# Optimization experiments

Hardware: AMD Instinct MI355X
Metric: run time of the kernel (lower is better)

Reference implementation:

```python
import math
import jax, jax.numpy as jnp
import numpy as np

B, T, C = 256, 200, 512
H = 8
N_ATTN = 512
HEAD = N_ATTN // H          # 64
ROT = HEAD // 2             # 32 (rotary_ndims = head_size * 0.5)
MAXLEN = 200
ITEM_NUM = 100000


def setup_inputs() -> dict:
    key = jax.random.key(0)
    ks = jax.random.split(key, 16)
    s = 0.02
    item_emb = jax.random.normal(ks[0], (ITEM_NUM + 1, C), jnp.float32) * s
    item_emb = item_emb.at[0].set(0.0)  # padding_idx=0
    inp = {
        "user_ids": jax.random.randint(ks[1], (B,), 0, 10000),
        "log_seqs": jax.random.randint(ks[2], (B, T), 0, ITEM_NUM + 1),
        "pos_seqs": jax.random.randint(ks[3], (B, T), 0, ITEM_NUM + 1),
        "neg_seqs": jax.random.randint(ks[4], (B, T), 0, ITEM_NUM + 1),
        "item_emb": item_emb,
        "time_w": 1.0 + jax.random.normal(ks[5], (H, MAXLEN), jnp.float32) * 0.1,
        "time_alpha": 1.0 + jax.random.normal(ks[6], (H, 1, MAXLEN), jnp.float32) * 0.1,
        "time_beta": 1.0 + jax.random.normal(ks[7], (H, MAXLEN, 1), jnp.float32) * 0.1,
        "time_gamma": 1.0 + jax.random.normal(ks[8], (MAXLEN, 1), jnp.float32) * 0.1,
        "Wq": jax.random.normal(ks[9], (N_ATTN, C), jnp.float32) * s,
        "bq": jnp.zeros((N_ATTN,), jnp.float32),
        "Wk": jax.random.normal(ks[10], (N_ATTN, C), jnp.float32) * s,
        "bk": jnp.zeros((N_ATTN,), jnp.float32),
        "Wv": jax.random.normal(ks[11], (N_ATTN, C), jnp.float32) * s,
        "bv": jnp.zeros((N_ATTN,), jnp.float32),
        "Wmix": jax.random.normal(ks[12], (H, H), jnp.float32) * (1.0 / math.sqrt(H)),
        "Wo": jax.random.normal(ks[13], (C, N_ATTN), jnp.float32) * s,
        "bo": jnp.zeros((C,), jnp.float32),
    }
    return inp


def _rotate_half(x):
    x1, x2 = x[..., : x.shape[-1] // 2], x[..., x.shape[-1] // 2 :]
    return jnp.concatenate((-x2, x1), axis=-1)


def _mha_pro(x_items, time_w, time_alpha, time_beta, time_gamma,
             Wq, bq, Wk, bk, Wv, bv, Wmix, Wo, bo):
    # x_items: [B, T, C]
    TT = MAXLEN
    # Toeplitz time-decay matrix built exactly like the torch pad/tile/reshape trick
    w = jnp.pad(time_w, ((0, 0), (0, TT)))          # [H, 2TT]
    w = jnp.tile(w, (1, TT))                         # [H, 2TT*TT]
    w = w[:, :-TT].reshape(H, TT, 2 * TT - 1)        # [H, TT, 2TT-1]
    w = w[:, :, TT - 1 :]                            # [H, TT, TT]
    w = w[:, :T, :T] * time_alpha[:, :, :T] * time_beta[:, :T, :]  # [H, T, T]

    # time_shift: shift first half of channels down by one token
    half = C // 2
    shifted = jnp.pad(x_items[:, :, :half], ((0, 0), (1, 0), (0, 0)))[:, :-1]
    x = jnp.concatenate([shifted, x_items[:, :, half:]], axis=-1)  # [B, T, C]

    q = (x @ Wq.T + bq).reshape(B, T, H, HEAD).transpose(0, 2, 1, 3)  # [B,H,T,D]
    k = (x @ Wk.T + bk).reshape(B, T, H, HEAD).transpose(0, 2, 1, 3)
    v = (x @ Wv.T + bv).reshape(B, T, H, HEAD).transpose(0, 2, 1, 3)

    # partial rotary on first ROT dims
    q_rot, q_pass = q[..., :ROT], q[..., ROT:]
    k_rot, k_pass = k[..., :ROT], k[..., ROT:]
    inv_freq = 1.0 / (10000.0 ** (jnp.arange(0, ROT, 2, dtype=jnp.float32) / ROT))
    freqs = jnp.arange(T, dtype=jnp.float32)[:, None] * inv_freq[None, :]  # [T, ROT/2]
    emb = jnp.concatenate((freqs, freqs), axis=-1)   # [T, ROT]
    cos, sin = jnp.cos(emb), jnp.sin(emb)
    q_rot = q_rot * cos + _rotate_half(q_rot) * sin
    k_rot = k_rot * cos + _rotate_half(k_rot) * sin
    q = jnp.concatenate((q_rot, q_pass), axis=-1)
    k = jnp.concatenate((k_rot, k_pass), axis=-1)

    att = jnp.einsum('bhtd,bhsd->bhts', q, k) * (1.0 / math.sqrt(HEAD))
    causal = jnp.tril(jnp.ones((T, T), bool))
    att = jnp.where(causal, att, -jnp.inf)
    att = jax.nn.softmax(att, axis=-1)
    att = att * w                                   # learned time-decay mask
    att = jnp.einsum('hg,bgts->bhts', Wmix, att)    # 1x1 conv across heads

    out = jnp.einsum('bhts,bhsd->bhtd', att, v)
    out = out.transpose(0, 2, 1, 3).reshape(B, T, N_ATTN)
    out = (out @ Wo.T + bo) * time_gamma[:T, :]
    return out


def reference(user_ids, log_seqs, pos_seqs, neg_seqs, item_emb,
              time_w, time_alpha, time_beta, time_gamma,
              Wq, bq, Wk, bk, Wv, bv, Wmix, Wo, bo):
    x_items = item_emb[log_seqs]                    # [B, T, C]
    log_feats = _mha_pro(x_items, time_w, time_alpha, time_beta, time_gamma,
                         Wq, bq, Wk, bk, Wv, bv, Wmix, Wo, bo)
    pos_embs = item_emb[pos_seqs]
    neg_embs = item_emb[neg_seqs]
    pos_logits = log_feats * pos_embs               # [B, T, C] (as in source)
    neg_logits = (log_feats * neg_embs).sum(axis=-1)  # [B, T]
    return pos_logits, neg_logits
```

## Files before the change

kernel.cpp:

```cpp
#include <hip/hip_runtime.h>

#define B_    256
#define T_    200
#define C_    512
#define H_    8
#define HEAD_ 64
#define M_    (B_ * T_)
#define POS_OUT_ (M_ * C_)
#define QK_ROWS_ 208
#define VT_PAD_  224
#define P_PAD_   208

typedef __attribute__((ext_vector_type(8))) _Float16 f16x8;
typedef __attribute__((ext_vector_type(4))) _Float16 f16x4;
typedef __attribute__((ext_vector_type(2))) _Float16 f16x2;
typedef __attribute__((ext_vector_type(4))) float f32x4;

__device__ __forceinline__ void gload16(const void* g, void* l) {
    __builtin_amdgcn_global_load_lds(
        (const __attribute__((address_space(1))) unsigned int*)g,
        (__attribute__((address_space(3))) unsigned int*)l, 16, 0, 0);
}

__global__ __launch_bounds__(256) void gather_shift_k(
    const float* __restrict__ emb, const int* __restrict__ logs,
    _Float16* __restrict__ x)
{
    int bt = blockIdx.x;
    int t  = bt % T_;
    int tid = threadIdx.x;
    int c  = tid * 2;
    _Float16* xr = x + (size_t)bt * C_;
    if (c < 256) {
        if (t == 0) {
            *(f16x2*)(xr + c) = (f16x2){(_Float16)0.0f, (_Float16)0.0f};
        } else {
            int id_prev = logs[bt - 1];
            float2 v = *(const float2*)(emb + (size_t)id_prev * C_ + c);
            *(f16x2*)(xr + c) = (f16x2){(_Float16)v.x, (_Float16)v.y};
        }
    } else {
        int id_cur = logs[bt];
        float2 v = *(const float2*)(emb + (size_t)id_cur * C_ + c);
        *(f16x2*)(xr + c) = (f16x2){(_Float16)v.x, (_Float16)v.y};
    }
}

__global__ __launch_bounds__(256) void convert_w_k(
    const float* __restrict__ Wq, const float* __restrict__ Wk,
    const float* __restrict__ Wv, const float* __restrict__ Wo,
    _Float16* __restrict__ dst)
{
    int idx = blockIdx.x * 256 + threadIdx.x;
    int mat = idx >> 16;
    int off = (idx & 65535) << 2;
    const float* src = (mat == 0) ? Wq : (mat == 1) ? Wk : (mat == 2) ? Wv : Wo;
    float4 v = *(const float4*)(src + off);
    f16x4 o = { (_Float16)v.x, (_Float16)v.y, (_Float16)v.z, (_Float16)v.w };
    *(f16x4*)(dst + ((size_t)mat << 18) + off) = o;
}

__global__ __launch_bounds__(256) void wtab_k(
    const float* __restrict__ tw, const float* __restrict__ ta,
    const float* __restrict__ tb, float* __restrict__ wtab)
{
    int idx = blockIdx.x * 256 + threadIdx.x;
    int g   = idx / (208 * 208);
    int rem = idx % (208 * 208);
    int t = rem / 208, s = rem % 208;
    int tt = min(t, 199), ss = min(s, 199);
    int wi = min(max(199 - tt + ss, 0), 199);
    wtab[idx] = tw[g * 200 + wi] * ta[g * 200 + ss] * tb[g * 200 + tt];
}

__global__ __launch_bounds__(256) void zero_pads_k(
    _Float16* __restrict__ Qb, _Float16* __restrict__ Kb,
    _Float16* __restrict__ Vt)
{
    int bh = blockIdx.x;
    int tid = threadIdx.x;
    for (int idx = tid; idx < 8 * 64; idx += 256) {
        Qb[(size_t)bh * QK_ROWS_ * 64 + 200 * 64 + idx] = (_Float16)0.0f;
        Kb[(size_t)bh * QK_ROWS_ * 64 + 200 * 64 + idx] = (_Float16)0.0f;
    }
    for (int idx = tid; idx < 64 * (VT_PAD_ - 200); idx += 256) {
        int d = idx / (VT_PAD_ - 200), s = 200 + idx % (VT_PAD_ - 200);
        Vt[(size_t)bh * 64 * VT_PAD_ + (size_t)d * VT_PAD_ + s] = (_Float16)0.0f;
    }
}

__global__ __launch_bounds__(256) void gemm_qkv_k(
    const _Float16* __restrict__ xh,
    const _Float16* __restrict__ Wh,
    const float* __restrict__ bq, const float* __restrict__ bk, const float* __restrict__ bv,
    _Float16* __restrict__ Qb, _Float16* __restrict__ Kb,
    _Float16* __restrict__ Vt,
    int nmt)
{
    int n = blockIdx.x;
    int mt, v;
    if ((nmt & 7) == 0) { int q8 = n & 7, i = n >> 3; mt = (i / 12) * 8 + q8; v = i % 12; }
    else               { mt = n / 12; v = n % 12; }
    int which = v >> 2;
    int nt    = v & 3;
    int m0    = mt * 128;
    const _Float16* Wm = Wh + ((size_t)(which * 4 + nt) * 128) * 512;
    const float* bias = (which == 0) ? bq : (which == 1) ? bk : bv;

    __shared__ _Float16 As[3][128 * 32];
    __shared__ _Float16 Bs[3][128 * 32];

    int tid  = threadIdx.x;
    int w    = tid >> 6, lane = tid & 63;
    int quad = lane >> 4, l15 = lane & 15;
    int wm   = w >> 1,    wn  = w & 1;
    int srow = lane >> 2, scg = lane & 3;
    int scg_src = scg ^ ((srow >> 1) & 3);
    int rq = (l15 >> 1) & 3;

    auto stage = [&](int buf, int k0) {
#pragma unroll
        for (int rr = 0; rr < 2; ++rr) {
            int seg = rr * 4 + w;
            int row = seg * 16 + srow;
            gload16(xh + (size_t)(m0 + row) * 512 + k0 + scg_src * 8, As[buf] + seg * 512);
            gload16(Wm + (size_t)row * 512 + k0 + scg_src * 8, Bs[buf] + seg * 512);
        }
    };

    f32x4 acc[4][4];
#pragma unroll
    for (int m = 0; m < 4; ++m)
#pragma unroll
        for (int nn = 0; nn < 4; ++nn) acc[m][nn] = (f32x4){0.f, 0.f, 0.f, 0.f};

    stage(0, 0);
    stage(1, 32);
#pragma unroll
    for (int s = 0; s < 16; ++s) {
        if (s < 15) asm volatile("s_waitcnt vmcnt(4)" ::: "memory");
        else        asm volatile("s_waitcnt vmcnt(0)" ::: "memory");
        __builtin_amdgcn_s_barrier();
        __builtin_amdgcn_sched_barrier(0);
        const _Float16* Ab = As[s % 3];
        const _Float16* Bb = Bs[s % 3];
        f16x8 af[4], bf[4];
#pragma unroll
        for (int m = 0; m < 4; ++m)
            af[m] = *(const f16x8*)(Ab + (wm * 4 + m) * 512 + l15 * 32 + (quad ^ rq) * 8);
#pragma unroll
        for (int nn = 0; nn < 4; ++nn)
            bf[nn] = *(const f16x8*)(Bb + (wn * 4 + nn) * 512 + l15 * 32 + (quad ^ rq) * 8);
        if (s <= 13) stage((s + 2) % 3, (s + 2) * 32);
#pragma unroll
        for (int m = 0; m < 4; ++m)
#pragma unroll
            for (int nn = 0; nn < 4; ++nn)
                acc[m][nn] = __builtin_amdgcn_mfma_f32_16x16x32_f16(af[m], bf[nn], acc[m][nn], 0, 0, 0);
    }

    int h = nt * 2 + wn;
    if (which < 2) {
        _Float16* dst = (which == 0) ? Qb : Kb;
        float sc = (which == 0) ? 0.125f : 1.0f;
        float invf = powf(10000.0f, -(float)l15 / 16.0f);
#pragma unroll
        for (int m = 0; m < 4; ++m) {
#pragma unroll
            for (int r = 0; r < 4; ++r) {
                int row = m0 + wm * 64 + m * 16 + quad * 4 + r;
                int bl = row / T_, t = row % T_;
                float sn, cs;
                __sincosf((float)t * invf, &sn, &cs);
                size_t base = ((size_t)(bl * 8 + h) * QK_ROWS_ + t) * 64;
                float av = acc[m][0][r] + bias[h * 64 + l15];
                float bv2 = acc[m][1][r] + bias[h * 64 + 16 + l15];
                dst[base + l15]      = (_Float16)((av * cs - bv2 * sn) * sc);
                dst[base + 16 + l15] = (_Float16)((bv2 * cs + av * sn) * sc);
                dst[base + 32 + l15] = (_Float16)((acc[m][2][r] + bias[h * 64 + 32 + l15]) * sc);
                dst[base + 48 + l15] = (_Float16)((acc[m][3][r] + bias[h * 64 + 48 + l15]) * sc);
            }
        }
    } else {
#pragma unroll
        for (int nn = 0; nn < 4; ++nn) {
            int ch = nn * 16 + l15;
            float bval = bias[h * 64 + ch];
#pragma unroll
            for (int m = 0; m < 4; ++m) {
                int r0 = m0 + wm * 64 + m * 16 + quad * 4;
                int t0v = r0 % T_;
                if (t0v <= 196) {
                    int bl = r0 / T_;
                    f16x4 v4 = {(_Float16)(acc[m][nn][0] + bval),
                                (_Float16)(acc[m][nn][1] + bval),
                                (_Float16)(acc[m][nn][2] + bval),
                                (_Float16)(acc[m][nn][3] + bval)};
                    *(f16x4*)(Vt + ((size_t)(bl * 8 + h) * 64 + ch) * VT_PAD_ + t0v) = v4;
                } else {
#pragma unroll
                    for (int r = 0; r < 4; ++r) {
                        int rw = r0 + r;
                        int bl = rw / T_, s = rw % T_;
                        Vt[((size_t)(bl * 8 + h) * 64 + ch) * VT_PAD_ + s] = (_Float16)(acc[m][nn][r] + bval);
                    }
                }
            }
        }
    }
}

__global__ __launch_bounds__(512) void attn_fused_k(
    const _Float16* __restrict__ Qb, const _Float16* __restrict__ Kb,
    const _Float16* __restrict__ Vt,
    const float* __restrict__ wtab,
    const float* __restrict__ wmix,
    _Float16* __restrict__ ao)
{
    int n    = blockIdx.x;
    int xcd  = n & 7, slot = n >> 3;
    int i_tile = slot % 13;
    int b      = (slot / 13) * 8 + xcd;

    int tid  = threadIdx.x;
    int wave = tid >> 6, lane = tid & 63;
    int quad = lane >> 4, l15 = lane & 15;
    int t0   = i_tile * 16;
    int nst  = i_tile + 1;
    int smax = nst * 16;

    __shared__ _Float16 Pt[8][16][P_PAD_];
    __shared__ float mixs[64];

    if (tid < 64) mixs[tid] = wmix[tid];
    __syncthreads();

    {
        int g = wave;
        const _Float16* Qg = Qb + (size_t)(b * 8 + g) * QK_ROWS_ * 64;
        const _Float16* Kg = Kb + (size_t)(b * 8 + g) * QK_ROWS_ * 64;
        f16x8 a0 = *(const f16x8*)(Qg + (size_t)(t0 + l15) * 64 + quad * 8);
        f16x8 a1 = *(const f16x8*)(Qg + (size_t)(t0 + l15) * 64 + quad * 8 + 32);

        f32x4 sf[13];
        __builtin_amdgcn_s_setprio(1);
#pragma unroll
        for (int st = 0; st < 13; ++st) if (st < nst) {
            f16x8 k0 = *(const f16x8*)(Kg + (size_t)(st * 16 + l15) * 64 + quad * 8);
            f16x8 k1 = *(const f16x8*)(Kg + (size_t)(st * 16 + l15) * 64 + quad * 8 + 32);
            f32x4 c = {0.f, 0.f, 0.f, 0.f};
            c = __builtin_amdgcn_mfma_f32_16x16x32_f16(a0, k0, c, 0, 0, 0);
            c = __builtin_amdgcn_mfma_f32_16x16x32_f16(a1, k1, c, 0, 0, 0);
            sf[st] = c;
        }
        __builtin_amdgcn_s_setprio(0);
        float inv[4];
#pragma unroll
        for (int r = 0; r < 4; ++r) {
            int t = t0 + quad * 4 + r;
            float sum = 0.f;
#pragma unroll
            for (int st = 0; st < 13; ++st) {
                if (st < nst - 1) {
                    float e = __expf(sf[st][r]); sf[st][r] = e; sum += e;
                } else if (st == nst - 1) {
                    int s = t0 + l15;
                    float e = (s <= t) ? __expf(sf[st][r]) : 0.f;
                    sf[st][r] = e; sum += e;
                }
            }
            sum += __shfl_xor(sum, 1);
            sum += __shfl_xor(sum, 2);
            sum += __shfl_xor(sum, 4);
            sum += __shfl_xor(sum, 8);
            inv[r] = 1.0f / sum;
        }
        const float* wg = wtab + ((size_t)g * 208 + t0) * 208;
#pragma unroll
        for (int st = 0; st < 13; ++st) if (st < nst) {
            int s = st * 16 + l15;
#pragma unroll
            for (int r = 0; r < 4; ++r) {
                int trow = quad * 4 + r;
                float wv = wg[trow * 208 + s];
                Pt[g][trow][s] = (_Float16)(sf[st][r] * inv[r] * wv);
            }
        }
    }
    __syncthreads();

    {
        f16x2 mx[64];
#pragma unroll
        for (int i = 0; i < 64; ++i) {
            _Float16 mh = (_Float16)mixs[i];
            mx[i] = (f16x2){mh, mh};
        }
        int nitems = smax << 3;
        for (int idx = tid; idx < nitems; idx += 512) {
            int tloc = idx & 15;
            int sp   = (idx >> 4) << 1;
            f16x2 pv[8];
#pragma unroll
            for (int g = 0; g < 8; ++g) pv[g] = *(const f16x2*)&Pt[g][tloc][sp];
#pragma unroll
            for (int ho = 0; ho < 8; ++ho) {
                f16x2 o = mx[ho * 8] * pv[0];
#pragma unroll
                for (int g = 1; g < 8; ++g) o += mx[ho * 8 + g] * pv[g];
                *(f16x2*)&Pt[ho][tloc][sp] = o;
            }
        }
    }
    __syncthreads();

    {
        int nk = (nst + 1) >> 1;
        int hda = wave;
        const _Float16* Vh = Vt + (size_t)(b * 8 + hda) * 64 * VT_PAD_;
        f32x4 c4[4];
#pragma unroll
        for (int n2 = 0; n2 < 4; ++n2) c4[n2] = (f32x4){0.f, 0.f, 0.f, 0.f};
        __builtin_amdgcn_s_setprio(1);
#pragma unroll
        for (int ks = 0; ks < 7; ++ks) if (ks < nk) {
            int cc = ks * 32 + quad * 8;
            bool oob = cc >= smax;
            int cl = oob ? 0 : cc;
            f16x8 a = *(const f16x8*)(&Pt[hda][l15][cl]);
            if (oob) {
#pragma unroll
                for (int j = 0; j < 8; ++j) a[j] = (_Float16)0.0f;
            }
#pragma unroll
            for (int n2 = 0; n2 < 4; ++n2) {
                f16x8 bb = *(const f16x8*)(Vh + (size_t)(n2 * 16 + l15) * VT_PAD_ + ks * 32 + quad * 8);
                c4[n2] = __builtin_amdgcn_mfma_f32_16x16x32_f16(a, bb, c4[n2], 0, 0, 0);
            }
        }
        __builtin_amdgcn_s_setprio(0);
#pragma unroll
        for (int n2 = 0; n2 < 4; ++n2)
#pragma unroll
            for (int r = 0; r < 4; ++r) {
                int t = t0 + quad * 4 + r;
                if (t < 200)
                    ao[((size_t)(b * T_ + t)) * 512 + hda * 64 + n2 * 16 + l15] = (_Float16)c4[n2][r];
            }
    }
}

__global__ __launch_bounds__(256) void gemm_out_k(
    const _Float16* __restrict__ Ah, const _Float16* __restrict__ Woh,
    const float* __restrict__ bo, const float* __restrict__ gamma,
    float* __restrict__ dst, int nmt)
{
    int n = blockIdx.x;
    int mt, nt;
    if ((nmt & 7) == 0) { int q8 = n & 7, i = n >> 3; mt = (i / 4) * 8 + q8; nt = i % 4; }
    else               { mt = n / 4; nt = n % 4; }
    int m0 = mt * 128;
    const _Float16* Wm = Woh + (size_t)nt * 128 * 512;

    __shared__ _Float16 As[3][128 * 32];
    __shared__ _Float16 Bs[3][128 * 32];

    int tid  = threadIdx.x;
    int w    = tid >> 6, lane = tid & 63;
    int quad = lane >> 4, l15 = lane & 15;
    int wm   = w >> 1,    wn  = w & 1;
    int srow = lane >> 2, scg = lane & 3;
    int scg_src = scg ^ ((srow >> 1) & 3);
    int rq = (l15 >> 1) & 3;

    auto stage = [&](int buf, int k0) {
#pragma unroll
        for (int rr = 0; rr < 2; ++rr) {
            int seg = rr * 4 + w;
            int row = seg * 16 + srow;
            gload16(Ah + (size_t)(m0 + row) * 512 + k0 + scg_src * 8, As[buf] + seg * 512);
            gload16(Wm + (size_t)row * 512 + k0 + scg_src * 8, Bs[buf] + seg * 512);
        }
    };

    f32x4 acc[4][4];
#pragma unroll
    for (int m = 0; m < 4; ++m)
#pragma unroll
        for (int nn = 0; nn < 4; ++nn) acc[m][nn] = (f32x4){0.f, 0.f, 0.f, 0.f};

    stage(0, 0);
    stage(1, 32);
#pragma unroll
    for (int s = 0; s < 16; ++s) {
        if (s < 15) asm volatile("s_waitcnt vmcnt(4)" ::: "memory");
        else        asm volatile("s_waitcnt vmcnt(0)" ::: "memory");
        __builtin_amdgcn_s_barrier();
        __builtin_amdgcn_sched_barrier(0);
        const _Float16* Ab = As[s % 3];
        const _Float16* Bb = Bs[s % 3];
        f16x8 af[4], bf[4];
#pragma unroll
        for (int m = 0; m < 4; ++m)
            af[m] = *(const f16x8*)(Ab + (wm * 4 + m) * 512 + l15 * 32 + (quad ^ rq) * 8);
#pragma unroll
        for (int nn = 0; nn < 4; ++nn)
            bf[nn] = *(const f16x8*)(Bb + (wn * 4 + nn) * 512 + l15 * 32 + (quad ^ rq) * 8);
        if (s <= 13) stage((s + 2) % 3, (s + 2) * 32);
#pragma unroll
        for (int m = 0; m < 4; ++m)
#pragma unroll
            for (int nn = 0; nn < 4; ++nn)
                acc[m][nn] = __builtin_amdgcn_mfma_f32_16x16x32_f16(af[m], bf[nn], acc[m][nn], 0, 0, 0);
    }

#pragma unroll
    for (int m = 0; m < 4; ++m)
#pragma unroll
        for (int nn = 0; nn < 4; ++nn)
#pragma unroll
            for (int r = 0; r < 4; ++r) {
                int row = m0 + wm * 64 + m * 16 + quad * 4 + r;
                int col = nt * 128 + wn * 64 + nn * 16 + l15;
                dst[(size_t)row * 512 + col] = (acc[m][nn][r] + bo[col]) * gamma[row % T_];
            }
}

__global__ __launch_bounds__(256) void logits_k(
    const float* __restrict__ lf, const float* __restrict__ emb,
    const int* __restrict__ pos, const int* __restrict__ neg,
    float* __restrict__ out, int bt0)
{
    int wid = threadIdx.x >> 6, lane = threadIdx.x & 63;
    int bt = blockIdx.x * 4 + wid;
    const float* l  = lf  + (size_t)bt * 512;
    const float* pe = emb + (size_t)pos[bt] * 512;
    const float* ne = emb + (size_t)neg[bt] * 512;
    float* po = out + (size_t)(bt0 + bt) * 512;
    float nacc = 0.f;
#pragma unroll
    for (int rep = 0; rep < 2; ++rep) {
        int i4 = (lane + rep * 64) * 4;
        float4 lv = *(const float4*)(l  + i4);
        float4 pv = *(const float4*)(pe + i4);
        float4 nv = *(const float4*)(ne + i4);
        float4 ov;
        ov.x = lv.x * pv.x; ov.y = lv.y * pv.y;
        ov.z = lv.z * pv.z; ov.w = lv.w * pv.w;
        *(float4*)(po + i4) = ov;
        nacc += lv.x * nv.x + lv.y * nv.y + lv.z * nv.z + lv.w * nv.w;
    }
#pragma unroll
    for (int off = 32; off >= 1; off >>= 1) nacc += __shfl_xor(nacc, off);
    if (lane == 0)
        out[(size_t)POS_OUT_ + bt0 + bt] = nacc;
}

extern "C" void kernel_launch(void* const* d_in, const int* in_sizes, int n_in,
                              void* d_out, int out_size, void* d_ws, size_t ws_size,
                              hipStream_t stream)
{
    const int* logs = (const int*)d_in[1];
    const int* pos  = (const int*)d_in[2];
    const int* neg  = (const int*)d_in[3];
    const float* emb = (const float*)d_in[4];
    const float* tw  = (const float*)d_in[5];
    const float* ta  = (const float*)d_in[6];
    const float* tb  = (const float*)d_in[7];
    const float* tg  = (const float*)d_in[8];
    const float* Wq  = (const float*)d_in[9];
    const float* bq  = (const float*)d_in[10];
    const float* Wk  = (const float*)d_in[11];
    const float* bk  = (const float*)d_in[12];
    const float* Wv  = (const float*)d_in[13];
    const float* bv  = (const float*)d_in[14];
    const float* wmix= (const float*)d_in[15];
    const float* Wo  = (const float*)d_in[16];
    const float* bo  = (const float*)d_in[17];

    const size_t PER_B = (size_t)T_ * C_ * 2
                       + (size_t)8 * QK_ROWS_ * 64 * 2
                       + (size_t)8 * QK_ROWS_ * 64 * 2
                       + (size_t)8 * 64 * VT_PAD_ * 2
                       + (size_t)T_ * C_ * 2
                       + (size_t)T_ * C_ * 4;
    const size_t SZ_WH = (size_t)4 * 512 * 512 * 2;
    const size_t SZ_WT = (size_t)8 * 208 * 208 * 4;

    int CB = (ws_size >= SZ_WH + SZ_WT + PER_B * B_) ? B_ : 32;
    int nch = B_ / CB;
    int CM = CB * T_;
    int NMT = CM / 128;

    char* p = (char*)d_ws;
    _Float16*       Wh   = (_Float16*)p;  p += SZ_WH;
    float*          wtab = (float*)p;     p += SZ_WT;
    _Float16*       xh   = (_Float16*)p;  p += (size_t)CM * C_ * 2;
    _Float16*       Qb   = (_Float16*)p;  p += (size_t)CB * 8 * QK_ROWS_ * 64 * 2;
    _Float16*       Kb   = (_Float16*)p;  p += (size_t)CB * 8 * QK_ROWS_ * 64 * 2;
    _Float16*       Vt   = (_Float16*)p;  p += (size_t)CB * 8 * 64 * VT_PAD_ * 2;
    _Float16*       aoh  = (_Float16*)p;  p += (size_t)CM * C_ * 2;
    float*          lf   = (float*)p;

    convert_w_k<<<1024, 256, 0, stream>>>(Wq, Wk, Wv, Wo, Wh);
    wtab_k<<<1352, 256, 0, stream>>>(tw, ta, tb, wtab);
    zero_pads_k<<<CB * 8, 256, 0, stream>>>(Qb, Kb, Vt);

    for (int c = 0; c < nch; ++c) {
        int bt0 = c * CM;
        gather_shift_k<<<CM, 256, 0, stream>>>(emb, logs + bt0, xh);
        gemm_qkv_k<<<NMT * 12, 256, 0, stream>>>(xh, Wh, bq, bk, bv, Qb, Kb, Vt, NMT);
        attn_fused_k<<<13 * CB, 512, 0, stream>>>(Qb, Kb, Vt, wtab, wmix, aoh);
        gemm_out_k<<<NMT * 4, 256, 0, stream>>>(aoh, Wh + (size_t)3 * 512 * 512, bo, tg, lf, NMT);
        logits_k<<<CM / 4, 256, 0, stream>>>(lf, emb, pos + bt0, neg + bt0, (float*)d_out, bt0);
    }
}
```

Measured before the change: 700.2 us.

## Fuse logits into output GEMM epilogue and prefetch K/V in attention

The separate logits kernel is removed. Its work moves into the gemm_out epilogue: pos logits are written directly, and neg logits are reduced with shuffles and accumulated with atomicAdd into an output region that a new kernel zeroes first. This avoids writing and re-reading the fp32 log_feats buffer. In the attention kernel the next K and V fragments are software-prefetched, the P LDS row padding changes, launch bounds gain a minimum-occupancy hint, and a barrier is dropped. The risks are less coalesced epilogue stores, atomic contention, higher register pressure, and a possible race on the shared mix weights.

Measured after the change: 689.5 us. About the same (-1.5%).

```diff
diff --git a/kernel.cpp b/kernel.cpp
--- a/kernel.cpp
+++ b/kernel.cpp
@@ -9,7 +9,7 @@
 #define POS_OUT_ (M_ * C_)
 #define QK_ROWS_ 208
 #define VT_PAD_  224
-#define P_PAD_   208
+#define P_PAD_   232
 
 typedef __attribute__((ext_vector_type(8))) _Float16 f16x8;
 typedef __attribute__((ext_vector_type(4))) _Float16 f16x4;
@@ -73,6 +73,11 @@
     wtab[idx] = tw[g * 200 + wi] * ta[g * 200 + ss] * tb[g * 200 + tt];
 }
 
+__global__ __launch_bounds__(256) void zero_neg_k(float* __restrict__ out)
+{
+    out[(size_t)POS_OUT_ + blockIdx.x * 256 + threadIdx.x] = 0.0f;
+}
+
 __global__ __launch_bounds__(256) void zero_pads_k(
     _Float16* __restrict__ Qb, _Float16* __restrict__ Kb,
     _Float16* __restrict__ Vt)
@@ -210,7 +215,7 @@
     }
 }
 
-__global__ __launch_bounds__(512) void attn_fused_k(
+__global__ __launch_bounds__(512, 4) void attn_fused_k(
     const _Float16* __restrict__ Qb, const _Float16* __restrict__ Kb,
     const _Float16* __restrict__ Vt,
     const float* __restrict__ wtab,
@@ -233,7 +238,6 @@
     __shared__ float mixs[64];
 
     if (tid < 64) mixs[tid] = wmix[tid];
-    __syncthreads();
 
     {
         int g = wave;
@@ -243,15 +247,21 @@
         f16x8 a1 = *(const f16x8*)(Qg + (size_t)(t0 + l15) * 64 + quad * 8 + 32);
 
         f32x4 sf[13];
+        f16x8 k0 = *(const f16x8*)(Kg + (size_t)l15 * 64 + quad * 8);
+        f16x8 k1 = *(const f16x8*)(Kg + (size_t)l15 * 64 + quad * 8 + 32);
         __builtin_amdgcn_s_setprio(1);
 #pragma unroll
         for (int st = 0; st < 13; ++st) if (st < nst) {
-            f16x8 k0 = *(const f16x8*)(Kg + (size_t)(st * 16 + l15) * 64 + quad * 8);
-            f16x8 k1 = *(const f16x8*)(Kg + (size_t)(st * 16 + l15) * 64 + quad * 8 + 32);
+            f16x8 nk0, nk1;
+            if (st + 1 < nst) {
+                nk0 = *(const f16x8*)(Kg + (size_t)((st + 1) * 16 + l15) * 64 + quad * 8);
+                nk1 = *(const f16x8*)(Kg + (size_t)((st + 1) * 16 + l15) * 64 + quad * 8 + 32);
+            }
             f32x4 c = {0.f, 0.f, 0.f, 0.f};
             c = __builtin_amdgcn_mfma_f32_16x16x32_f16(a0, k0, c, 0, 0, 0);
             c = __builtin_amdgcn_mfma_f32_16x16x32_f16(a1, k1, c, 0, 0, 0);
             sf[st] = c;
+            k0 = nk0; k1 = nk1;
         }
         __builtin_amdgcn_s_setprio(0);
         float inv[4];
@@ -321,9 +331,18 @@
         f32x4 c4[4];
 #pragma unroll
         for (int n2 = 0; n2 < 4; ++n2) c4[n2] = (f32x4){0.f, 0.f, 0.f, 0.f};
+        f16x8 vb[4], vn[4];
+#pragma unroll
+        for (int n2 = 0; n2 < 4; ++n2)
+            vb[n2] = *(const f16x8*)(Vh + (size_t)(n2 * 16 + l15) * VT_PAD_ + quad * 8);
         __builtin_amdgcn_s_setprio(1);
 #pragma unroll
         for (int ks = 0; ks < 7; ++ks) if (ks < nk) {
+            if (ks + 1 < nk) {
+#pragma unroll
+                for (int n2 = 0; n2 < 4; ++n2)
+                    vn[n2] = *(const f16x8*)(Vh + (size_t)(n2 * 16 + l15) * VT_PAD_ + (ks + 1) * 32 + quad * 8);
+            }
             int cc = ks * 32 + quad * 8;
             bool oob = cc >= smax;
             int cl = oob ? 0 : cc;
@@ -333,10 +352,10 @@
                 for (int j = 0; j < 8; ++j) a[j] = (_Float16)0.0f;
             }
 #pragma unroll
-            for (int n2 = 0; n2 < 4; ++n2) {
-                f16x8 bb = *(const f16x8*)(Vh + (size_t)(n2 * 16 + l15) * VT_PAD_ + ks * 32 + quad * 8);
-                c4[n2] = __builtin_amdgcn_mfma_f32_16x16x32_f16(a, bb, c4[n2], 0, 0, 0);
-            }
+            for (int n2 = 0; n2 < 4; ++n2)
+                c4[n2] = __builtin_amdgcn_mfma_f32_16x16x32_f16(a, vb[n2], c4[n2], 0, 0, 0);
+#pragma unroll
+            for (int n2 = 0; n2 < 4; ++n2) vb[n2] = vn[n2];
         }
         __builtin_amdgcn_s_setprio(0);
 #pragma unroll
@@ -353,7 +372,9 @@
 __global__ __launch_bounds__(256) void gemm_out_k(
     const _Float16* __restrict__ Ah, const _Float16* __restrict__ Woh,
     const float* __restrict__ bo, const float* __restrict__ gamma,
-    float* __restrict__ dst, int nmt)
+    const float* __restrict__ emb, const int* __restrict__ pos,
+    const int* __restrict__ neg, float* __restrict__ out,
+    int bt0, int nmt)
 {
     int n = blockIdx.x;
     int mt, nt;
@@ -415,45 +436,31 @@
     }
 
 #pragma unroll
-    for (int m = 0; m < 4; ++m)
-#pragma unroll
-        for (int nn = 0; nn < 4; ++nn)
-#pragma unroll
-            for (int r = 0; r < 4; ++r) {
-                int row = m0 + wm * 64 + m * 16 + quad * 4 + r;
+    for (int m = 0; m < 4; ++m) {
+#pragma unroll
+        for (int r = 0; r < 4; ++r) {
+            int row = m0 + wm * 64 + m * 16 + quad * 4 + r;
+            float gg = gamma[row % T_];
+            int pr = pos[row], nr = neg[row];
+            const float* pe = emb + (size_t)pr * 512;
+            const float* ne = emb + (size_t)nr * 512;
+            float* po = out + (size_t)(bt0 + row) * 512;
+            float s = 0.f;
+#pragma unroll
+            for (int nn = 0; nn < 4; ++nn) {
                 int col = nt * 128 + wn * 64 + nn * 16 + l15;
-                dst[(size_t)row * 512 + col] = (acc[m][nn][r] + bo[col]) * gamma[row % T_];
-            }
-}
-
-__global__ __launch_bounds__(256) void logits_k(
-    const float* __restrict__ lf, const float* __restrict__ emb,
-    const int* __restrict__ pos, const int* __restrict__ neg,
-    float* __restrict__ out, int bt0)
-{
-    int wid = threadIdx.x >> 6, lane = threadIdx.x & 63;
-    int bt = blockIdx.x * 4 + wid;
-    const float* l  = lf  + (size_t)bt * 512;
-    const float* pe = emb + (size_t)pos[bt] * 512;
-    const float* ne = emb + (size_t)neg[bt] * 512;
-    float* po = out + (size_t)(bt0 + bt) * 512;
-    float nacc = 0.f;
-#pragma unroll
-    for (int rep = 0; rep < 2; ++rep) {
-        int i4 = (lane + rep * 64) * 4;
-        float4 lv = *(const float4*)(l  + i4);
-        float4 pv = *(const float4*)(pe + i4);
-        float4 nv = *(const float4*)(ne + i4);
-        float4 ov;
-        ov.x = lv.x * pv.x; ov.y = lv.y * pv.y;
-        ov.z = lv.z * pv.z; ov.w = lv.w * pv.w;
-        *(float4*)(po + i4) = ov;
-        nacc += lv.x * nv.x + lv.y * nv.y + lv.z * nv.z + lv.w * nv.w;
-    }
-#pragma unroll
-    for (int off = 32; off >= 1; off >>= 1) nacc += __shfl_xor(nacc, off);
-    if (lane == 0)
-        out[(size_t)POS_OUT_ + bt0 + bt] = nacc;
+                float val = (acc[m][nn][r] + bo[col]) * gg;
+                po[col] = val * pe[col];
+                s += val * ne[col];
+            }
+            s += __shfl_xor(s, 1);
+            s += __shfl_xor(s, 2);
+            s += __shfl_xor(s, 4);
+            s += __shfl_xor(s, 8);
+            if (l15 == 0)
+                atomicAdd(out + (size_t)POS_OUT_ + bt0 + row, s);
+        }
+    }
 }
 
 extern "C" void kernel_launch(void* const* d_in, const int* in_sizes, int n_in,
@@ -482,8 +489,7 @@
                        + (size_t)8 * QK_ROWS_ * 64 * 2
                        + (size_t)8 * QK_ROWS_ * 64 * 2
                        + (size_t)8 * 64 * VT_PAD_ * 2
-                       + (size_t)T_ * C_ * 2
-                       + (size_t)T_ * C_ * 4;
+                       + (size_t)T_ * C_ * 2;
     const size_t SZ_WH = (size_t)4 * 512 * 512 * 2;
     const size_t SZ_WT = (size_t)8 * 208 * 208 * 4;
 
@@ -499,11 +505,11 @@
     _Float16*       Qb   = (_Float16*)p;  p += (size_t)CB * 8 * QK_ROWS_ * 64 * 2;
     _Float16*       Kb   = (_Float16*)p;  p += (size_t)CB * 8 * QK_ROWS_ * 64 * 2;
     _Float16*       Vt   = (_Float16*)p;  p += (size_t)CB * 8 * 64 * VT_PAD_ * 2;
-    _Float16*       aoh  = (_Float16*)p;  p += (size_t)CM * C_ * 2;
-    float*          lf   = (float*)p;
+    _Float16*       aoh  = (_Float16*)p;
 
     convert_w_k<<<1024, 256, 0, stream>>>(Wq, Wk, Wv, Wo, Wh);
     wtab_k<<<1352, 256, 0, stream>>>(tw, ta, tb, wtab);
+    zero_neg_k<<<M_ / 256, 256, 0, stream>>>((float*)d_out);
     zero_pads_k<<<CB * 8, 256, 0, stream>>>(Qb, Kb, Vt);
 
     for (int c = 0; c < nch; ++c) {
@@ -511,7 +517,7 @@
         gather_shift_k<<<CM, 256, 0, stream>>>(emb, logs + bt0, xh);
         gemm_qkv_k<<<NMT * 12, 256, 0, stream>>>(xh, Wh, bq, bk, bv, Qb, Kb, Vt, NMT);
         attn_fused_k<<<13 * CB, 512, 0, stream>>>(Qb, Kb, Vt, wtab, wmix, aoh);
-        gemm_out_k<<<NMT * 4, 256, 0, stream>>>(aoh, Wh + (size_t)3 * 512 * 512, bo, tg, lf, NMT);
-        logits_k<<<CM / 4, 256, 0, stream>>>(lf, emb, pos + bt0, neg + bt0, (float*)d_out, bt0);
-    }
-}
+        gemm_out_k<<<NMT * 4, 256, 0, stream>>>(aoh, Wh + (size_t)3 * 512 * 512, bo, tg,
+                                                emb, pos + bt0, neg + bt0, (float*)d_out, bt0, NMT);
+    }
+}
```
